# Performance work log

Hardware: AMD Instinct MI355X
Metric: run time of the kernel (lower is better)

## Reference

```python
import jax, jax.numpy as jnp
import numpy as np

B, S, D, H = 2, 512, 512, 8
HD = D // H  # 64


def setup_inputs() -> dict:
    key = jax.random.key(0)
    ks = jax.random.split(key, 14)
    sd = 1.0 / np.sqrt(D)
    sh = 1.0 / np.sqrt(HD)
    return {
        "query": jax.random.normal(ks[0], (B, S, D), jnp.float32),
        "key_": jax.random.normal(ks[1], (B, S, D), jnp.float32),
        "value": jax.random.normal(ks[2], (B, S, D), jnp.float32),
        "Wq": jax.random.uniform(ks[3], (D, D), jnp.float32, -sd, sd),
        "bq": jax.random.uniform(ks[4], (D,), jnp.float32, -sd, sd),
        "Wk": jax.random.uniform(ks[5], (D, D), jnp.float32, -sd, sd),
        "bk": jax.random.uniform(ks[6], (D,), jnp.float32, -sd, sd),
        "Wv": jax.random.uniform(ks[7], (D, D), jnp.float32, -sd, sd),
        "bv": jax.random.uniform(ks[8], (D,), jnp.float32, -sd, sd),
        "Wo": jax.random.uniform(ks[9], (D, D), jnp.float32, -sd, sd),
        "bo": jax.random.uniform(ks[10], (D,), jnp.float32, -sd, sd),
        "Aq": jax.random.uniform(ks[11], (HD, HD), jnp.float32, -sh, sh),
        "Ak": jax.random.uniform(ks[12], (HD, HD), jnp.float32, -sh, sh),
        "av": jax.random.normal(ks[13], (HD,), jnp.float32) * sh,
    }


def _heads(x):
    b, s, _ = x.shape
    return x.reshape(b, s, H, HD).transpose(0, 2, 1, 3)  # [b,h,s,hd]


def reference(query, key_, value, Wq, bq, Wk, bk, Wv, bv, Wo, bo, Aq, Ak, av):
    q = _heads(query @ Wq + bq)   # [b,h,q,hd]
    k = _heads(key_ @ Wk + bk)    # [b,h,k,hd]
    v = _heads(value @ Wv + bv)   # [b,h,k,hd]
    # additive (Bahdanau-style) scores: tanh(add_q(q)[:,:,:,None]+add_k(k)[:,:,None]) . av
    q_term = (q @ Aq)[:, :, :, None, :]   # [b,h,q,1,hd]
    k_term = (k @ Ak)[:, :, None, :, :]   # [b,h,1,k,hd]
    scores = jnp.einsum('bhqkd,d->bhqk', jnp.tanh(q_term + k_term), av)
    attn_weights = jax.nn.softmax(scores, axis=-1)  # dropout is identity at eval
    ctx = jnp.einsum('bhqk,bhkd->bhqd', attn_weights, v)
    b, _, s, _ = ctx.shape
    ctx = ctx.transpose(0, 2, 1, 3).reshape(b, s, D)
    out = ctx @ Wo + bo
    return out, attn_weights
```

## Files before the change

### kernel.cpp

```cpp
#include <hip/hip_runtime.h>
#include <math.h>

#define Bb 2
#define Ss 512
#define Dd 512
#define Hh 8
#define HDd 64
#define BS (Bb*Ss)

#if __has_builtin(__builtin_amdgcn_exp2f)
#define EXP2F(x) __builtin_amdgcn_exp2f(x)
#else
#define EXP2F(x) exp2f(x)
#endif
#if __has_builtin(__builtin_amdgcn_rcpf)
#define RCPF(x) __builtin_amdgcn_rcpf(x)
#else
#define RCPF(x) (1.0f/(x))
#endif

typedef float v4f __attribute__((ext_vector_type(4)));
typedef short v8s __attribute__((ext_vector_type(8)));

struct HL { short h, l; };

__device__ __forceinline__ HL split1(float x) {
  unsigned u = __builtin_bit_cast(unsigned, x);
  unsigned h = (u + 0x7fffu + ((u >> 16) & 1u)) >> 16;
  float hf = __builtin_bit_cast(float, h << 16);
  float lo = x - hf;
  unsigned ul = __builtin_bit_cast(unsigned, lo);
  unsigned l = (ul + 0x7fffu + ((ul >> 16) & 1u)) >> 16;
  HL r; r.h = (short)h; r.l = (short)l;
  return r;
}

__device__ __forceinline__ void split8p(const float* __restrict__ xp, v8s& ah, v8s& al) {
#pragma unroll
  for (int j = 0; j < 8; j++) {
    const HL r = split1(xp[j]);
    ah[j] = r.h; al[j] = r.l;
  }
}

__device__ __forceinline__ void split8v(float4 x0, float4 x1, v8s& ah, v8s& al) {
  HL r;
  r = split1(x0.x); ah[0] = r.h; al[0] = r.l;
  r = split1(x0.y); ah[1] = r.h; al[1] = r.l;
  r = split1(x0.z); ah[2] = r.h; al[2] = r.l;
  r = split1(x0.w); ah[3] = r.h; al[3] = r.l;
  r = split1(x1.x); ah[4] = r.h; al[4] = r.l;
  r = split1(x1.y); ah[5] = r.h; al[5] = r.l;
  r = split1(x1.z); ah[6] = r.h; al[6] = r.l;
  r = split1(x1.w); ah[7] = r.h; al[7] = r.l;
}

#if __has_builtin(__builtin_amdgcn_global_load_lds)
__device__ __forceinline__ void gl2lds16(const float* g, float* l) {
  __builtin_amdgcn_global_load_lds(
      (const __attribute__((address_space(1))) void*)g,
      (__attribute__((address_space(3))) void*)l, 16, 0, 0);
}
#else
__device__ __forceinline__ void gl2lds16(const float* g, float* l) {
  const int lane = threadIdx.x & 63;
  *(float4*)((char*)l + lane * 16) = *(const float4*)g;
}
#endif

__global__ __launch_bounds__(256) void qkv_all(
    const float* __restrict__ Xq, const float* __restrict__ Xk, const float* __restrict__ Xv,
    const float* __restrict__ Wq, const float* __restrict__ Wk, const float* __restrict__ Wv,
    const float* __restrict__ Wo,
    const float* __restrict__ bq, const float* __restrict__ bk, const float* __restrict__ bv,
    const float* __restrict__ bo,
    const float* __restrict__ Aq, const float* __restrict__ Ak,
    float* __restrict__ EQ, float* __restrict__ EKt, float* __restrict__ Vw,
    short* __restrict__ WoPk, float* __restrict__ outp)
{
  __shared__ __align__(16) short fragH[2][4][64][8];
  __shared__ __align__(16) short fragL[2][4][64][8];
  __shared__ float qs[64][68];
  __shared__ float qs2[16][260];

  const int z = blockIdx.z;
  const float* X    = (z == 0) ? Xq : (z == 1) ? Xk : Xv;
  const float* W    = (z == 0) ? Wq : (z == 1) ? Wk : Wv;
  const float* bias = (z == 0) ? bq : (z == 1) ? bk : bv;
  const int tid = threadIdx.x, l = tid & 63, w = tid >> 6;
  const int lm = l & 15, lq = l >> 4;
  const int h = blockIdx.x;
  const int r0 = blockIdx.y * 64;

  v4f acc[4] = {{0.f,0.f,0.f,0.f},{0.f,0.f,0.f,0.f},{0.f,0.f,0.f,0.f},{0.f,0.f,0.f,0.f}};
  const float* xrow = X + (size_t)(r0 + w * 16 + lm) * Dd + lq * 8;

  for (int kt = 0; kt < 16; ++kt) {
    const int buf = kt & 1;
    const float4 xa0 = *(const float4*)&xrow[kt * 32];
    const float4 xa1 = *(const float4*)&xrow[kt * 32 + 4];
    {
      v8s hh, ll;
#pragma unroll
      for (int j = 0; j < 8; j++) {
        const float x = W[(size_t)(kt * 32 + lq * 8 + j) * Dd + h * 64 + w * 16 + lm];
        const HL r = split1(x);
        hh[j] = r.h; ll[j] = r.l;
      }
      *(v8s*)&fragH[buf][w][l][0] = hh;
      *(v8s*)&fragL[buf][w][l][0] = ll;
    }
    __syncthreads();
    v8s ah, al;
    split8v(xa0, xa1, ah, al);
#pragma unroll
    for (int t = 0; t < 4; t++) {
      const v8s bh = *(const v8s*)&fragH[buf][t][l][0];
      const v8s bl = *(const v8s*)&fragL[buf][t][l][0];
      acc[t] = __builtin_amdgcn_mfma_f32_16x16x32_bf16(ah, bh, acc[t], 0, 0, 0);
      acc[t] = __builtin_amdgcn_mfma_f32_16x16x32_bf16(ah, bl, acc[t], 0, 0, 0);
      acc[t] = __builtin_amdgcn_mfma_f32_16x16x32_bf16(al, bh, acc[t], 0, 0, 0);
    }
  }

  if (z == 2) {
#pragma unroll
    for (int t = 0; t < 4; t++) {
      const int n = h * 64 + t * 16 + lm;
      const float bvv = bias[n];
#pragma unroll
      for (int r = 0; r < 4; r++)
        Vw[(size_t)(r0 + w * 16 + lq * 4 + r) * Dd + n] = acc[t][r] + bvv;
    }
    {
      const int tau = (blockIdx.y * 8 + h) * 4 + w;
      const int nt = tau >> 4, kt = tau & 15;
      v8s hh, ll;
#pragma unroll
      for (int j = 0; j < 8; j++) {
        const float x = Wo[(size_t)(kt * 32 + lq * 8 + j) * Dd + nt * 16 + lm];
        const HL r = split1(x);
        hh[j] = r.h; ll[j] = r.l;
      }
      *(v8s*)&WoPk[((size_t)tau * 64 + l) * 16 + 0] = hh;
      *(v8s*)&WoPk[((size_t)tau * 64 + l) * 16 + 8] = ll;
    }
    for (int i = tid; i < 4096; i += 256) {
      const int rr2 = i >> 6, cc = i & 63;
      outp[(size_t)(r0 + rr2) * Dd + h * 64 + cc] = bo[h * 64 + cc];
    }
    return;
  }

#pragma unroll
  for (int t = 0; t < 4; t++) {
    const int n = h * 64 + t * 16 + lm;
    const float bvv = bias[n];
#pragma unroll
    for (int r = 0; r < 4; r++)
      qs[w * 16 + lq * 4 + r][t * 16 + lm] = acc[t][r] + bvv;
  }
  __syncthreads();

  const float* Am = (z == 0) ? Aq : Ak;
  v4f a2[4] = {{0.f,0.f,0.f,0.f},{0.f,0.f,0.f,0.f},{0.f,0.f,0.f,0.f},{0.f,0.f,0.f,0.f}};
#pragma unroll
  for (int kt2 = 0; kt2 < 2; ++kt2) {
    v8s ah, al;
    split8p(&qs[w * 16 + lm][kt2 * 32 + lq * 8], ah, al);
#pragma unroll
    for (int t2 = 0; t2 < 4; t2++) {
      v8s bh, bl;
#pragma unroll
      for (int j = 0; j < 8; j++) {
        const float x = Am[(kt2 * 32 + lq * 8 + j) * HDd + t2 * 16 + lm]
                        * 2.885390081777927f;
        const HL r = split1(x);
        bh[j] = r.h; bl[j] = r.l;
      }
      a2[t2] = __builtin_amdgcn_mfma_f32_16x16x32_bf16(ah, bh, a2[t2], 0, 0, 0);
      a2[t2] = __builtin_amdgcn_mfma_f32_16x16x32_bf16(ah, bl, a2[t2], 0, 0, 0);
      a2[t2] = __builtin_amdgcn_mfma_f32_16x16x32_bf16(al, bh, a2[t2], 0, 0, 0);
    }
  }

  if (z == 0) {
#pragma unroll
    for (int t2 = 0; t2 < 4; t2++)
#pragma unroll
      for (int rr = 0; rr < 4; rr++)
        EQ[(size_t)(r0 + w * 16 + lq * 4 + rr) * Dd + h * 64 + t2 * 16 + lm] = EXP2F(a2[t2][rr]);
  } else {
#pragma unroll
    for (int t2 = 0; t2 < 4; t2++)
#pragma unroll
      for (int rr = 0; rr < 4; rr++)
        qs2[4 * t2 + (lm >> 2)][(w * 16 + lq * 4 + rr) * 4 + (lm & 3)] = EXP2F(a2[t2][rr]);
    __syncthreads();
    const int b = r0 >> 9;
    const size_t base = (size_t)(b * 8 + h) * 16 * 2048 + (size_t)(r0 & 511) * 4;
#pragma unroll
    for (int i = 0; i < 4; i++) {
      const int f = i * 1024 + tid * 4;
      const int dt = f >> 8, c = f & 255;
      *(float4*)&EKt[base + (size_t)dt * 2048 + c] = *(const float4*)&qs2[dt][c];
    }
  }
}

__device__ __forceinline__ float grp4(v4f e, v4f ek, v4f av4) {
  const v4f one = {1.f, 1.f, 1.f, 1.f};
  const v4f den = e * ek + one;
  const float AB = den.x * den.y;
  const float CD = den.z * den.w;
  const float n1 = __builtin_fmaf(av4.y, den.x, av4.x * den.y);
  const float n2 = __builtin_fmaf(av4.w, den.z, av4.z * den.w);
  const float N = __builtin_fmaf(n2, AB, n1 * CD);
  return N * RCPF(AB * CD);
}

__global__ __launch_bounds__(256) void attn_kernel(
    const float* __restrict__ EQ, const float* __restrict__ EKt,
    const float* __restrict__ V, const float* __restrict__ av,
    const short* __restrict__ WoPk,
    float* __restrict__ attnW, float* __restrict__ outp)
{
  __shared__ __align__(16) float uni[8256];
  __shared__ __align__(16) float eq_s[16][64];
  __shared__ float avn[64];

  const int tid = threadIdx.x, l = tid & 63, w = tid >> 6;
  const int lm = l & 15, lq = l >> 4;
  const int q0 = blockIdx.x * 16;
  const int bh = blockIdx.y;
  const int b = bh >> 3, h = bh & 7;

  {
    const float* eqg = EQ + (size_t)(b * Ss + q0 + w * 4 + lq) * Dd
                       + h * HDd + lm * 4;
    gl2lds16(eqg, &eq_s[w * 4][0]);
  }
  if (tid < 64) avn[tid] = -2.f * av[tid];

  const float* ekbase = EKt + (size_t)bh * 16 * 2048;
  gl2lds16(ekbase + w * 512 + l * 4, &uni[w * 512]);
  gl2lds16(ekbase + w * 512 + 256 + l * 4, &uni[w * 512 + 256]);
  __syncthreads();

  const int qg = w * 4;
  float a[4][8];
#pragma unroll
  for (int j = 0; j < 4; j++)
#pragma unroll
    for (int kg = 0; kg < 8; kg++) a[j][kg] = 0.f;

#pragma unroll 1
  for (int dt = 0; dt < 16; ++dt) {
    const int cb = (dt & 1) * 2048;
    const int nb = 2048 - cb;
    const int dtn = (dt < 15) ? dt + 1 : 15;
    gl2lds16(ekbase + (size_t)dtn * 2048 + w * 512 + l * 4, &uni[nb + w * 512]);
    gl2lds16(ekbase + (size_t)dtn * 2048 + w * 512 + 256 + l * 4, &uni[nb + w * 512 + 256]);

    const v4f av4 = *(const v4f*)&avn[dt * 4];
    const v4f e0 = *(const v4f*)&eq_s[qg + 0][dt * 4];
    const v4f e1 = *(const v4f*)&eq_s[qg + 1][dt * 4];
    const v4f e2 = *(const v4f*)&eq_s[qg + 2][dt * 4];
    const v4f e3 = *(const v4f*)&eq_s[qg + 3][dt * 4];
#pragma unroll
    for (int kg = 0; kg < 8; kg++) {
      const v4f ek = *(const v4f*)&uni[cb + kg * 256 + l * 4];
      a[0][kg] += grp4(e0, ek, av4);
      a[1][kg] += grp4(e1, ek, av4);
      a[2][kg] += grp4(e2, ek, av4);
      a[3][kg] += grp4(e3, ek, av4);
    }
    __syncthreads();
  }

#pragma unroll
  for (int j = 0; j < 4; j++) {
    float m = -1e30f;
#pragma unroll
    for (int kg = 0; kg < 8; kg++) m = fmaxf(m, a[j][kg]);
#pragma unroll
    for (int off = 32; off >= 1; off >>= 1) m = fmaxf(m, __shfl_xor(m, off, 64));
    float s = 0.f;
#pragma unroll
    for (int kg = 0; kg < 8; kg++) {
      a[j][kg] = EXP2F((a[j][kg] - m) * 1.4426950408889634f);
      s += a[j][kg];
    }
#pragma unroll
    for (int off = 32; off >= 1; off >>= 1) s += __shfl_xor(s, off, 64);
    const float inv = RCPF(s);
    float* arow = attnW + ((size_t)bh * Ss + q0 + qg + j) * Ss;
#pragma unroll
    for (int kg = 0; kg < 8; kg++) {
      const float wv = a[j][kg] * inv;
      uni[(qg + j) * 516 + kg * 64 + l] = wv;
      arow[kg * 64 + l] = wv;
    }
  }
  __syncthreads();

  {
    const int cq = tid >> 4;
    const int dq = (tid & 15) * 4;
    const float* vb = V + (size_t)b * Ss * Dd + h * HDd + dq;
    const float* scr = &uni[cq * 516];
    v4f o = {0.f, 0.f, 0.f, 0.f};
    for (int kk = 0; kk < Ss; kk += 2) {
      const float2 wv = *(const float2*)&scr[kk];
      const v4f v0 = *(const v4f*)&vb[(size_t)kk * Dd];
      const v4f v1 = *(const v4f*)&vb[(size_t)(kk + 1) * Dd];
      o += wv.x * v0 + wv.y * v1;
    }
    *(v4f*)&eq_s[cq][dq] = o;
  }
  __syncthreads();

  {
    v4f oacc[8];
#pragma unroll
    for (int i = 0; i < 8; i++) oacc[i] = (v4f){0.f, 0.f, 0.f, 0.f};
#pragma unroll
    for (int kt2 = 0; kt2 < 2; ++kt2) {
      v8s ah, al;
      split8p(&eq_s[lm][kt2 * 32 + lq * 8], ah, al);
#pragma unroll
      for (int n8 = 0; n8 < 8; n8++) {
        const int tau = (w * 8 + n8) * 16 + 2 * h + kt2;
        const size_t bi = ((size_t)tau * 64 + l) * 16;
        const v8s bh = *(const v8s*)&WoPk[bi + 0];
        const v8s bl = *(const v8s*)&WoPk[bi + 8];
        oacc[n8] = __builtin_amdgcn_mfma_f32_16x16x32_bf16(ah, bh, oacc[n8], 0, 0, 0);
        oacc[n8] = __builtin_amdgcn_mfma_f32_16x16x32_bf16(ah, bl, oacc[n8], 0, 0, 0);
        oacc[n8] = __builtin_amdgcn_mfma_f32_16x16x32_bf16(al, bh, oacc[n8], 0, 0, 0);
      }
    }
#pragma unroll
    for (int n8 = 0; n8 < 8; n8++) {
      const int n = (w * 8 + n8) * 16 + lm;
#pragma unroll
      for (int r = 0; r < 4; r++)
        atomicAdd(&outp[(size_t)(b * Ss + q0 + lq * 4 + r) * Dd + n], oacc[n8][r]);
    }
  }
}

extern "C" void kernel_launch(void* const* d_in, const int* in_sizes, int n_in,
                              void* d_out, int out_size, void* d_ws, size_t ws_size,
                              hipStream_t stream) {
  (void)in_sizes; (void)n_in; (void)out_size; (void)ws_size;
  const float* query = (const float*)d_in[0];
  const float* key_  = (const float*)d_in[1];
  const float* value = (const float*)d_in[2];
  const float* Wq    = (const float*)d_in[3];
  const float* bq    = (const float*)d_in[4];
  const float* Wk    = (const float*)d_in[5];
  const float* bk    = (const float*)d_in[6];
  const float* Wv    = (const float*)d_in[7];
  const float* bv    = (const float*)d_in[8];
  const float* Wo    = (const float*)d_in[9];
  const float* bo    = (const float*)d_in[10];
  const float* Aq    = (const float*)d_in[11];
  const float* Ak    = (const float*)d_in[12];
  const float* av    = (const float*)d_in[13];

  float* outp = (float*)d_out;
  float* attn = outp + (size_t)BS * Dd;

  float* ws  = (float*)d_ws;
  float* EQ  = ws;
  float* EKt = ws + (size_t)BS * Dd;
  float* Vw  = ws + 2 * (size_t)BS * Dd;
  short* WoPk = (short*)(ws + 3 * (size_t)BS * Dd);

  qkv_all<<<dim3(8, 16, 3), 256, 0, stream>>>(query, key_, value,
      Wq, Wk, Wv, Wo, bq, bk, bv, bo, Aq, Ak, EQ, EKt, Vw, WoPk, outp);
  attn_kernel<<<dim3(32, 16), 256, 0, stream>>>(EQ, EKt, Vw, av,
      WoPk, attn, outp);
}
```

Baseline: 170.8 us.

## Split PV over key ranges per wave with register reuse of V loads, stagger atomics

```diff
diff --git a/kernel.cpp b/kernel.cpp
--- a/kernel.cpp
+++ b/kernel.cpp
@@ -227,6 +227,7 @@
 {
   __shared__ __align__(16) float uni[8256];
   __shared__ __align__(16) float eq_s[16][64];
+  __shared__ __align__(16) float ctx_s[16][68];
   __shared__ float avn[64];
 
   const int tid = threadIdx.x, l = tid & 63, w = tid >> 6;
@@ -305,18 +306,43 @@
   __syncthreads();
 
   {
-    const int cq = tid >> 4;
-    const int dq = (tid & 15) * 4;
-    const float* vb = V + (size_t)b * Ss * Dd + h * HDd + dq;
-    const float* scr = &uni[cq * 516];
-    v4f o = {0.f, 0.f, 0.f, 0.f};
-    for (int kk = 0; kk < Ss; kk += 2) {
-      const float2 wv = *(const float2*)&scr[kk];
-      const v4f v0 = *(const v4f*)&vb[(size_t)kk * Dd];
-      const v4f v1 = *(const v4f*)&vb[(size_t)(kk + 1) * Dd];
-      o += wv.x * v0 + wv.y * v1;
-    }
-    *(v4f*)&eq_s[cq][dq] = o;
+    const int rg = (tid >> 4) & 3;
+    const int dq = tid & 15;
+    const int k0 = w * 128;
+    const float* scr0 = &uni[(4 * rg + 0) * 516];
+    const float* scr1 = &uni[(4 * rg + 1) * 516];
+    const float* scr2 = &uni[(4 * rg + 2) * 516];
+    const float* scr3 = &uni[(4 * rg + 3) * 516];
+    const float* vb = V + (size_t)b * Ss * Dd + h * HDd + dq * 4;
+    v4f o0 = {0.f,0.f,0.f,0.f}, o1 = {0.f,0.f,0.f,0.f};
+    v4f o2 = {0.f,0.f,0.f,0.f}, o3 = {0.f,0.f,0.f,0.f};
+    for (int kk = k0; kk < k0 + 128; kk += 2) {
+      const float2 w0 = *(const float2*)&scr0[kk];
+      const float2 w1 = *(const float2*)&scr1[kk];
+      const float2 w2 = *(const float2*)&scr2[kk];
+      const float2 w3 = *(const float2*)&scr3[kk];
+      const v4f va = *(const v4f*)&vb[(size_t)kk * Dd];
+      const v4f vz = *(const v4f*)&vb[(size_t)(kk + 1) * Dd];
+      o0 += w0.x * va + w0.y * vz;
+      o1 += w1.x * va + w1.y * vz;
+      o2 += w2.x * va + w2.y * vz;
+      o3 += w3.x * va + w3.y * vz;
+    }
+    __syncthreads();
+    *(v4f*)&uni[w * 1024 + (4 * rg + 0) * 64 + dq * 4] = o0;
+    *(v4f*)&uni[w * 1024 + (4 * rg + 1) * 64 + dq * 4] = o1;
+    *(v4f*)&uni[w * 1024 + (4 * rg + 2) * 64 + dq * 4] = o2;
+    *(v4f*)&uni[w * 1024 + (4 * rg + 3) * 64 + dq * 4] = o3;
+  }
+  __syncthreads();
+  {
+    const int e = tid * 4;
+    const int r = e >> 6, c = e & 63;
+    v4f s0 = *(const v4f*)&uni[e];
+    s0 += *(const v4f*)&uni[1024 + e];
+    s0 += *(const v4f*)&uni[2048 + e];
+    s0 += *(const v4f*)&uni[3072 + e];
+    *(v4f*)&ctx_s[r][c] = s0;
   }
   __syncthreads();
 
@@ -327,10 +353,11 @@
 #pragma unroll
     for (int kt2 = 0; kt2 < 2; ++kt2) {
       v8s ah, al;
-      split8p(&eq_s[lm][kt2 * 32 + lq * 8], ah, al);
+      split8p(&ctx_s[lm][kt2 * 32 + lq * 8], ah, al);
 #pragma unroll
       for (int n8 = 0; n8 < 8; n8++) {
-        const int tau = (w * 8 + n8) * 16 + 2 * h + kt2;
+        const int n8i = (n8 + h) & 7;
+        const int tau = (w * 8 + n8i) * 16 + 2 * h + kt2;
         const size_t bi = ((size_t)tau * 64 + l) * 16;
         const v8s bh = *(const v8s*)&WoPk[bi + 0];
         const v8s bl = *(const v8s*)&WoPk[bi + 8];
@@ -341,7 +368,8 @@
     }
 #pragma unroll
     for (int n8 = 0; n8 < 8; n8++) {
-      const int n = (w * 8 + n8) * 16 + lm;
+      const int n8i = (n8 + h) & 7;
+      const int n = (w * 8 + n8i) * 16 + lm;
 #pragma unroll
       for (int r = 0; r < 4; r++)
         atomicAdd(&outp[(size_t)(b * Ss + q0 + lq * 4 + r) * Dd + n], oacc[n8][r]);
```

New measurement: 161.9 us. 1.05x faster.
